# Optimization experiments

Hardware: AMD Instinct MI355X
Metric: run time of the kernel (lower is better)

The kernel has to match this reference:

```python
import jax, jax.numpy as jnp
import numpy as np

VX, VY, VT = 3.0, 3.0, 1.0
PCX, PCY, PCT = 346.0, 260.0, 200.0
GX, GY = 116, 87  # ceil(346/3), ceil(260/3)
B = 4
NSEG = B * GX * GY  # dense pillar id space (replaces torch.unique)
EPS = 1e-3  # BatchNorm1d eps


def _bn_swish(h, gamma, beta):
    # BatchNorm1d (training-mode batch stats) + Swish
    mu = jnp.mean(h, axis=0)
    var = jnp.var(h, axis=0)
    h = (h - mu) * jax.lax.rsqrt(var + EPS) * gamma + beta
    return h * jax.nn.sigmoid(h)


def _voxelize(points):
    # points: [N,5] = (batch_idx, x, y, t, polarity)
    cx = jnp.floor(points[:, 1] / VX).astype(jnp.int32)
    cy = jnp.floor(points[:, 2] / VY).astype(jnp.int32)
    bi = points[:, 0].astype(jnp.int32)
    inv = (bi * GX + cx) * GY + cy  # dense pillar id == unq_inv into dense grid
    xyz = points[:, 1:4]
    cnt = jax.ops.segment_sum(jnp.ones_like(xyz[:, 0]), inv, num_segments=NSEG)
    mean = jax.ops.segment_sum(xyz, inv, num_segments=NSEG) / jnp.maximum(cnt, 1.0)[:, None]
    f_cluster = xyz - mean[inv]
    cxy = jnp.stack([cx, cy], axis=1).astype(points.dtype)
    vsz = jnp.array([VX, VY], points.dtype)
    f_center = points[:, 1:3] - (cxy * vsz + (vsz - 1.0) / 2.0)
    feats = jnp.concatenate([points[:, 1:5], f_cluster, f_center], axis=1)  # [N,9]
    scale = jnp.array([PCX, PCY, PCT, 1.0, VX, VY, PCT, VX, VY], points.dtype)
    feats = feats / scale
    return feats[:, :4], inv, cnt  # module only keeps first 4 feature columns


def _resize_bilinear_ac(x, Ho, Wo):
    # F.interpolate(mode='bilinear', align_corners=True)
    _, _, H, W = x.shape
    ys = jnp.linspace(0.0, H - 1.0, Ho)
    xs = jnp.linspace(0.0, W - 1.0, Wo)
    y0 = jnp.floor(ys).astype(jnp.int32); y1 = jnp.minimum(y0 + 1, H - 1)
    x0 = jnp.floor(xs).astype(jnp.int32); x1 = jnp.minimum(x0 + 1, W - 1)
    wy = (ys - y0.astype(x.dtype))[None, None, :, None]
    wx = (xs - x0.astype(x.dtype))[None, None, None, :]
    xh = x[:, :, y0, :] * (1.0 - wy) + x[:, :, y1, :] * wy
    return xh[:, :, :, x0] * (1.0 - wx) + xh[:, :, :, x1] * wx


def setup_inputs() -> dict:
    key = jax.random.key(0)
    ks = jax.random.split(key, 8)
    N = 1_000_000
    b = jax.random.randint(ks[0], (N, 1), 0, B).astype(jnp.float32)
    x = jax.random.uniform(ks[1], (N, 1)) * 345.9
    y = jax.random.uniform(ks[2], (N, 1)) * 259.9
    t = jax.random.uniform(ks[3], (N, 1)) * 199.9
    p = jax.random.randint(ks[4], (N, 1), 0, 2).astype(jnp.float32)
    points = jnp.concatenate([b, x, y, t, p], axis=1)
    fus = jax.random.normal(ks[5], (B, 3, 224, 224), jnp.float32)
    W0 = jax.random.normal(ks[6], (4, 32), jnp.float32) * 0.1
    g0 = jnp.ones(32, jnp.float32); b0 = jnp.zeros(32, jnp.float32)
    W1 = jax.random.normal(ks[7], (64, 128), jnp.float32) * 0.05
    g1 = jnp.ones(128, jnp.float32); b1 = jnp.zeros(128, jnp.float32)
    return {"fus": fus, "points": points, "W0": W0, "g0": g0, "b0": b0,
            "W1": W1, "g1": g1, "b1": b1}


def reference(fus, points, W0, g0, b0, W1, g1, b1):
    feats, inv, cnt = _voxelize(points)
    # PFNLayer 0 (not last): units = 64//2 = 32, concat per-pillar max
    h0 = _bn_swish(feats @ W0, g0, b0)
    m0 = jax.ops.segment_max(h0, inv, num_segments=NSEG)
    x1 = jnp.concatenate([h0, m0[inv]], axis=1)  # [N,64]
    # PFNLayer 1 (last): units = 128, returns broadcast per-pillar max
    h1 = _bn_swish(x1 @ W1, g1, b1)
    m1 = jax.ops.segment_max(h1, inv, num_segments=NSEG)  # [NSEG,128]
    # final scatter_max over the broadcast max equals m1 on occupied pillars;
    # spconv .dense() zero-fills empty pillars
    occ = cnt > 0
    dense = jnp.where(occ[:, None], m1, 0.0)
    dense = dense.reshape(B, GX, GY, -1).transpose(0, 3, 2, 1)  # [B,C,GY,GX]
    return _resize_bilinear_ac(dense, 224, 224)
```

## Files before the change

kernel.cpp:

```cpp
#include <hip/hip_runtime.h>
#include <cmath>

#define NPTS   1000000
#define GXD    116
#define GYD    87
#define NB     4
#define NSEG   40368
#define OUTN   25690112

#define OFF_INV    0
#define OFF_CNT    2000000
#define OFF_OFFS   2050000
#define OFF_FILL   2100000
#define OFF_STATS  2150000
#define OFF_BN0    2158500
#define OFF_FRAG   2158592
#define OFF_MINP   2170000
#define OFF_MAXP   7340000
#define OFF_SPTS   12510000

typedef __attribute__((ext_vector_type(8))) short short8v;
typedef __attribute__((ext_vector_type(4))) float float4v;

union Frag {
  unsigned u[4];
  int4 i4;
  short8v v;
};

__device__ __forceinline__ float fastrcp(float x) { return __builtin_amdgcn_rcpf(x); }
__device__ __forceinline__ float swishf(float z) { return z * fastrcp(1.0f + __expf(-z)); }
__device__ __forceinline__ unsigned fbits(float x) { return __builtin_bit_cast(unsigned, x); }
__device__ __forceinline__ float ubf(unsigned x) { return __builtin_bit_cast(float, x); }

__device__ __forceinline__ void bfsplit2(float x0, float x1, unsigned& hi, unsigned& lo) {
  unsigned h0b = fbits(x0) & 0xffff0000u;
  unsigned h1b = fbits(x1) & 0xffff0000u;
  hi = (h0b >> 16) | h1b;
  float l0 = x0 - ubf(h0b), l1 = x1 - ubf(h1b);
  lo = (fbits(l0) >> 16) | (fbits(l1) & 0xffff0000u);
}

__global__ __launch_bounds__(256) void k_init(int* __restrict__ cnt, int* __restrict__ fill,
                                              float* __restrict__ stats) {
  int i = blockIdx.x * 256 + threadIdx.x;
  if (i < NSEG) { cnt[i] = 0; fill[i] = 0; }
  if (i < 8224) stats[i] = 0.0f;
}

__global__ __launch_bounds__(256) void k_point1(const float* __restrict__ pts,
                                                int* __restrict__ inv,
                                                int* __restrict__ cnt,
                                                float* __restrict__ Sg) {
  float acc[14];
  #pragma unroll
  for (int q = 0; q < 14; ++q) acc[q] = 0.0f;
  const float i346 = 1.0f / 346.0f, i260 = 1.0f / 260.0f, i200 = 1.0f / 200.0f;
  const int stride = gridDim.x * 256;
  for (int i = blockIdx.x * 256 + threadIdx.x; i < NPTS; i += stride) {
    float b = pts[i*5];
    float4 v = *(const float4*)(pts + i*5 + 1);
    float x = v.x, y = v.y, t = v.z, p = v.w;
    int cx = (int)floorf(x / 3.0f);
    int cy = (int)floorf(y / 3.0f);
    int bi = (int)b;
    if (cx >= 0 && cx < GXD && cy >= 0 && cy < GYD && bi >= 0 && bi < NB) {
      int iv = (bi*GXD + cx)*GYD + cy;
      inv[i] = iv;
      atomicAdd(&cnt[iv], 1);
    } else {
      inv[i] = -1;
    }
    float f0 = x*i346, f1 = y*i260, f2 = t*i200, f3 = p;
    acc[0]+=f0; acc[1]+=f1; acc[2]+=f2; acc[3]+=f3;
    acc[4]+=f0*f0; acc[5]+=f0*f1; acc[6]+=f0*f2; acc[7]+=f0*f3;
    acc[8]+=f1*f1; acc[9]+=f1*f2; acc[10]+=f1*f3;
    acc[11]+=f2*f2; acc[12]+=f2*f3; acc[13]+=f3*f3;
  }
  __shared__ float lds[4*14];
  int lane = threadIdx.x & 63, wave = threadIdx.x >> 6;
  #pragma unroll
  for (int q = 0; q < 14; ++q) {
    float v = acc[q];
    #pragma unroll
    for (int d = 32; d > 0; d >>= 1) v += __shfl_down(v, d, 64);
    if (lane == 0) lds[wave*14 + q] = v;
  }
  __syncthreads();
  if (threadIdx.x < 14) {
    float v = lds[threadIdx.x] + lds[14+threadIdx.x] + lds[28+threadIdx.x] + lds[42+threadIdx.x];
    atomicAdd(&Sg[threadIdx.x], v);
  }
}

__global__ __launch_bounds__(1024) void k_scan(const int* __restrict__ cnt,
                                               int* __restrict__ offs,
                                               const float* __restrict__ S,
                                               float* __restrict__ bn0,
                                               int4* __restrict__ frag,
                                               const float* __restrict__ W0,
                                               const float* __restrict__ g0,
                                               const float* __restrict__ b0,
                                               const float* __restrict__ W1) {
  __shared__ int wtot[16];
  const int tid = threadIdx.x;
  if (tid < 32) {
    const float invN = 1.0f / (float)NPTS;
    float w0 = W0[tid], w1 = W0[32+tid], w2 = W0[64+tid], w3 = W0[96+tid];
    float mu = (S[0]*w0 + S[1]*w1 + S[2]*w2 + S[3]*w3) * invN;
    float e2 = (S[4]*w0*w0 + S[8]*w1*w1 + S[11]*w2*w2 + S[13]*w3*w3
              + 2.0f*(S[5]*w0*w1 + S[6]*w0*w2 + S[7]*w0*w3
                    + S[9]*w1*w2 + S[10]*w1*w3 + S[12]*w2*w3)) * invN;
    float var = e2 - mu*mu;
    float a = rsqrtf(var + 1e-3f) * g0[tid];
    bn0[tid] = a;
    bn0[32+tid] = b0[tid] - mu*a;
  }
  if (tid < 512) {
    const int t = tid >> 6, ln = tid & 63;
    const int qq = ln >> 4, rr = ln & 15;
    Frag fh, fl, gh, gl;
    #pragma unroll
    for (int d = 0; d < 4; ++d) {
      int row = 8*qq + 2*d, col = 16*t + rr;
      bfsplit2(W1[row*128 + col],      W1[(row+1)*128 + col],  fh.u[d], fl.u[d]);
      bfsplit2(W1[(32+row)*128 + col], W1[(33+row)*128 + col], gh.u[d], gl.u[d]);
    }
    frag[tid]        = fh.i4;
    frag[512 + tid]  = fl.i4;
    frag[1024 + tid] = gh.i4;
    frag[1536 + tid] = gl.i4;
  }
  const int CH = 40;
  const int base = tid * CH;
  int loc[CH];
  int s = 0;
  #pragma unroll
  for (int i = 0; i < CH; ++i) {
    int v = (base + i < NSEG) ? cnt[base + i] : 0;
    loc[i] = s; s += v;
  }
  int inc = s;
  const int lane = tid & 63, wv = tid >> 6;
  #pragma unroll
  for (int d = 1; d < 64; d <<= 1) {
    int t = __shfl_up(inc, d, 64);
    if (lane >= d) inc += t;
  }
  if (lane == 63) wtot[wv] = inc;
  __syncthreads();
  if (tid == 0) {
    int run = 0;
    #pragma unroll
    for (int w = 0; w < 16; ++w) { int t = wtot[w]; wtot[w] = run; run += t; }
    offs[NSEG] = run;
  }
  __syncthreads();
  int ex = wtot[wv] + (inc - s);
  #pragma unroll
  for (int i = 0; i < CH; ++i)
    if (base + i < NSEG) offs[base + i] = ex + loc[i];
}

__global__ __launch_bounds__(256) void k_scatter(const float* __restrict__ pts,
                                                 const int* __restrict__ inv,
                                                 const int* __restrict__ offs,
                                                 int* __restrict__ fill,
                                                 float4* __restrict__ sp) {
  int i = blockIdx.x * 256 + threadIdx.x;
  if (i >= NPTS) return;
  int iv = inv[i];
  if (iv < 0) return;
  float4 v = *(const float4*)(pts + i*5 + 1);
  int pos = offs[iv] + atomicAdd(&fill[iv], 1);
  sp[pos] = v;
}

__global__ __launch_bounds__(256) void k_seg(const float4* __restrict__ sp,
                                             const int* __restrict__ offs,
                                             const float* __restrict__ W0,
                                             const float* __restrict__ bn0,
                                             const int4* __restrict__ frags,
                                             float* __restrict__ minp,
                                             float* __restrict__ maxp,
                                             float* __restrict__ stats) {
  __shared__ int4 fragLDS[1536];
  __shared__ float redS[4][16][16];
  const int tid = threadIdx.x;
  const int wave = tid >> 6, lane = tid & 63;
  const int q = lane >> 4, r = lane & 15;

  short8v Bhi[8];
  #pragma unroll
  for (int t = 0; t < 8; ++t) {
    Frag f; f.i4 = frags[t*64 + lane];
    Bhi[t] = f.v;
  }
  for (int i = tid; i < 1536; i += 256) fragLDS[i] = frags[512 + i];

  const float i346 = 1.0f/346.0f, i260 = 1.0f/260.0f, i200 = 1.0f/200.0f;
  float wax[8], way[8], wat[8], wap[8], wc0[8];
  #pragma unroll
  for (int j = 0; j < 8; ++j) {
    int ch = 8*q + j;
    float a0 = bn0[ch];
    wax[j] = W0[ch]    * (i346 * a0);
    way[j] = W0[32+ch] * (i260 * a0);
    wat[j] = W0[64+ch] * (i200 * a0);
    wap[j] = W0[96+ch] * a0;
    wc0[j] = bn0[32+ch];
  }
  __syncthreads();

  float gsum[8], gssq[8];
  #pragma unroll
  for (int t = 0; t < 8; ++t) { gsum[t] = 0.f; gssq[t] = 0.f; }

  const int w = blockIdx.x*4 + wave;
  const int qn = NSEG >> 13;
  const int rm = NSEG - (qn << 13);
  const int s0 = w*qn + (w < rm ? w : rm);
  const int scnt = qn + (w < rm ? 1 : 0);

  for (int s = s0; s < s0 + scnt; ++s) {
    const int off = offs[s], pend = offs[s+1];
    const int n = pend - off;
    if (n <= 0) continue;
    const int ngroups = (n + 15) >> 4;
    float m0r[8], mn[8], mx[8], su[8], sq[8];
    #pragma unroll
    for (int t = 0; t < 8; ++t) {
      m0r[t] = -1e30f; mn[t] = 1e30f; mx[t] = -1e30f; su[t] = 0.f; sq[t] = 0.f;
    }
    float4 P = sp[off + (r < n ? r : 0)];
    for (int g = 0; g < ngroups; ++g) {
      int slot1 = (g+1)*16 + r;
      float4 Pn = sp[off + (slot1 < n ? slot1 : 0)];

      float h0v[8];
      #pragma unroll
      for (int j = 0; j < 8; ++j) {
        float pre = fmaf(P.x, wax[j], fmaf(P.y, way[j], fmaf(P.z, wat[j], fmaf(P.w, wap[j], wc0[j]))));
        float h = swishf(pre);
        h0v[j] = h;
        m0r[j] = fmaxf(m0r[j], h);
      }
      Frag ah, al;
      #pragma unroll
      for (int d = 0; d < 4; ++d)
        bfsplit2(h0v[2*d], h0v[2*d+1], ah.u[d], al.u[d]);

      const int rem = n - g*16;
      #pragma unroll
      for (int t = 0; t < 8; ++t) {
        Frag fb; fb.i4 = fragLDS[t*64 + lane];
        float4v acc = {0.f, 0.f, 0.f, 0.f};
        acc = __builtin_amdgcn_mfma_f32_16x16x32_bf16(ah.v, Bhi[t], acc, 0, 0, 0);
        acc = __builtin_amdgcn_mfma_f32_16x16x32_bf16(ah.v, fb.v,   acc, 0, 0, 0);
        acc = __builtin_amdgcn_mfma_f32_16x16x32_bf16(al.v, Bhi[t], acc, 0, 0, 0);
        if (rem >= 16) {
          #pragma unroll
          for (int i = 0; i < 4; ++i) {
            float z = acc[i];
            mn[t] = fminf(mn[t], z); mx[t] = fmaxf(mx[t], z);
            su[t] += z; sq[t] = fmaf(z, z, sq[t]);
          }
        } else {
          #pragma unroll
          for (int i = 0; i < 4; ++i) {
            float z = acc[i];
            mn[t] = fminf(mn[t], z); mx[t] = fmaxf(mx[t], z);
            float zz = (4*q + i < rem) ? z : 0.f;
            su[t] += zz; sq[t] = fmaf(zz, zz, sq[t]);
          }
        }
      }
      P = Pn;
    }

    #pragma unroll
    for (int j = 0; j < 8; ++j) {
      float v = m0r[j];
      v = fmaxf(v, __shfl_xor(v, 1, 64));
      v = fmaxf(v, __shfl_xor(v, 2, 64));
      v = fmaxf(v, __shfl_xor(v, 4, 64));
      v = fmaxf(v, __shfl_xor(v, 8, 64));
      m0r[j] = v;
    }
    Frag mh, ml;
    #pragma unroll
    for (int d = 0; d < 4; ++d)
      bfsplit2(m0r[2*d], m0r[2*d+1], mh.u[d], ml.u[d]);
    float c[8];
    #pragma unroll
    for (int t = 0; t < 8; ++t) {
      Frag gh; gh.i4 = fragLDS[512 + t*64 + lane];
      Frag gl; gl.i4 = fragLDS[1024 + t*64 + lane];
      float4v cacc = {0.f, 0.f, 0.f, 0.f};
      cacc = __builtin_amdgcn_mfma_f32_16x16x32_bf16(mh.v, gh.v, cacc, 0, 0, 0);
      cacc = __builtin_amdgcn_mfma_f32_16x16x32_bf16(mh.v, gl.v, cacc, 0, 0, 0);
      cacc = __builtin_amdgcn_mfma_f32_16x16x32_bf16(ml.v, gh.v, cacc, 0, 0, 0);
      c[t] = cacc[0];
    }
    #pragma unroll
    for (int t = 0; t < 8; ++t) {
      mn[t] = fminf(mn[t], __shfl_xor(mn[t], 16, 64));
      mn[t] = fminf(mn[t], __shfl_xor(mn[t], 32, 64));
      mx[t] = fmaxf(mx[t], __shfl_xor(mx[t], 16, 64));
      mx[t] = fmaxf(mx[t], __shfl_xor(mx[t], 32, 64));
      su[t] += __shfl_xor(su[t], 16, 64);
      su[t] += __shfl_xor(su[t], 32, 64);
      sq[t] += __shfl_xor(sq[t], 16, 64);
      sq[t] += __shfl_xor(sq[t], 32, 64);
      float nf = (float)n;
      gsum[t] += su[t] + nf * c[t];
      gssq[t] += sq[t] + 2.0f*c[t]*su[t] + nf*c[t]*c[t];
    }
    if (lane < 16) {
      #pragma unroll
      for (int t = 0; t < 8; ++t) {
        minp[(16*t + r)*NSEG + s] = mn[t] + c[t];
        maxp[(16*t + r)*NSEG + s] = mx[t] + c[t];
      }
    }
  }
  if (lane < 16) {
    #pragma unroll
    for (int t = 0; t < 8; ++t) {
      redS[wave][r][t]     = gsum[t];
      redS[wave][r][8 + t] = gssq[t];
    }
  }
  __syncthreads();
  if (wave == 0 && lane < 16) {
    const int cpy = blockIdx.x & 15;
    float* sb = stats + 16 + 512*cpy;
    #pragma unroll
    for (int t = 0; t < 8; ++t) {
      float s0v = redS[0][r][t]   + redS[1][r][t]   + redS[2][r][t]   + redS[3][r][t];
      float q0v = redS[0][r][8+t] + redS[1][r][8+t] + redS[2][r][8+t] + redS[3][r][8+t];
      atomicAdd(&sb[16*t + r], s0v);
      atomicAdd(&sb[256 + 16*t + r], q0v);
    }
  }
}

__global__ __launch_bounds__(256) void k_plane(const float* __restrict__ minp,
                                               const float* __restrict__ maxp,
                                               const int* __restrict__ offs,
                                               const float* __restrict__ stats,
                                               const float* __restrict__ g1,
                                               const float* __restrict__ b1,
                                               float* __restrict__ out) {
  __shared__ float plane[87*117];
  __shared__ float ab[2];
  const int c = blockIdx.x & 127;
  const int b = blockIdx.x >> 7;
  const int tid = threadIdx.x;
  if (tid == 0) {
    float s = 0.f, q2 = 0.f;
    #pragma unroll
    for (int cpy = 0; cpy < 16; ++cpy) {
      s  += stats[16 + 512*cpy + c];
      q2 += stats[16 + 512*cpy + 256 + c];
    }
    const float invN = 1.0f / (float)NPTS;
    float mu = s * invN;
    float var = q2 * invN - mu*mu;
    float a = rsqrtf(var + 1e-3f) * g1[c];
    ab[0] = a;
    ab[1] = b1[c] - mu*a;
  }
  __syncthreads();
  const float a = ab[0], bb = ab[1];
  const int sBase = b * (GXD*GYD);
  const float* mnp = minp + c*NSEG + sBase;
  const float* mxp = maxp + c*NSEG + sBase;
  for (int i = tid; i < GXD*GYD; i += 256) {
    int gx = i / GYD, gy = i - gx*GYD;
    float m = 0.0f;
    int s = sBase + i;
    if (offs[s+1] - offs[s] > 0) {
      float zl = fmaf(a, mnp[i], bb);
      float zh = fmaf(a, mxp[i], bb);
      m = fmaxf(swishf(zl), swishf(zh));
    }
    plane[gy*117 + gx] = m;
  }
  __syncthreads();
  float* op = out + (size_t)blockIdx.x * (224*224);
  for (int o4 = tid; o4 < 224*56; o4 += 256) {
    int xq = o4 % 56;
    int yo = o4 / 56;
    float ys = (float)yo * (86.0f/223.0f);
    float yf = floorf(ys); int y0 = (int)yf; int y1 = min(y0+1, 86); float wy = ys - yf;
    const float* p0 = plane + y0*117;
    const float* p1 = plane + y1*117;
    float res[4];
    #pragma unroll
    for (int gph = 0; gph < 4; ++gph) {
      int xo = xq*4 + gph;
      float xs = (float)xo * (115.0f/223.0f);
      float xf = floorf(xs); int x0 = (int)xf; int x1 = min(x0+1, 115); float wx = xs - xf;
      float c0v = p0[x0]*(1.0f-wy) + p1[x0]*wy;
      float c1v = p0[x1]*(1.0f-wy) + p1[x1]*wy;
      res[gph] = c0v*(1.0f-wx) + c1v*wx;
    }
    *(float4*)&op[yo*224 + xq*4] = make_float4(res[0], res[1], res[2], res[3]);
  }
}

extern "C" void kernel_launch(void* const* d_in, const int* in_sizes, int n_in,
                              void* d_out, int out_size, void* d_ws, size_t ws_size,
                              hipStream_t stream) {
  const float* pts = (const float*)d_in[1];
  const float* W0  = (const float*)d_in[2];
  const float* g0  = (const float*)d_in[3];
  const float* b0  = (const float*)d_in[4];
  const float* W1  = (const float*)d_in[5];
  const float* g1  = (const float*)d_in[6];
  const float* b1  = (const float*)d_in[7];
  float* out = (float*)d_out;
  int*   wsi = (int*)d_ws;
  float* wsf = (float*)d_ws;

  k_init<<<158, 256, 0, stream>>>(wsi+OFF_CNT, wsi+OFF_FILL, wsf+OFF_STATS);
  k_point1<<<256, 256, 0, stream>>>(pts, wsi+OFF_INV, wsi+OFF_CNT, wsf+OFF_STATS);
  k_scan<<<1, 1024, 0, stream>>>(wsi+OFF_CNT, wsi+OFF_OFFS, wsf+OFF_STATS, wsf+OFF_BN0,
                                 (int4*)(wsf+OFF_FRAG), W0, g0, b0, W1);
  k_scatter<<<(NPTS+255)/256, 256, 0, stream>>>(pts, wsi+OFF_INV, wsi+OFF_OFFS,
                                                wsi+OFF_FILL, (float4*)(wsf+OFF_SPTS));
  k_seg<<<2048, 256, 0, stream>>>((const float4*)(wsf+OFF_SPTS), wsi+OFF_OFFS, W0,
                                  wsf+OFF_BN0, (const int4*)(wsf+OFF_FRAG),
                                  wsf+OFF_MINP, wsf+OFF_MAXP, wsf+OFF_STATS);
  k_plane<<<NB*128, 256, 0, stream>>>(wsf+OFF_MINP, wsf+OFF_MAXP, wsi+OFF_OFFS,
                                      wsf+OFF_STATS, g1, b1, out);
}
```

Baseline: 430.9 us.

## Stage per-segment min/max in LDS and write contiguous runs; use min3/max3

The segment kernel now hands each block a contiguous range of segments, with its four waves interleaved across that range, instead of giving each wave its own contiguous range. Per-segment min/max results are staged in shared memory and then written cooperatively, so stores into the channel-major min/max planes form contiguous runs instead of scattered single-element writes. Grid size doubles to 4096 blocks. The statistic accumulation uses v_min3/v_max3 inline asm and pairwise sums, which changes the order of float additions slightly.

Result: slower. 458.0 us (+6.3%).

```diff
diff --git a/kernel.cpp b/kernel.cpp
--- a/kernel.cpp
+++ b/kernel.cpp
@@ -7,6 +7,9 @@
 #define NB     4
 #define NSEG   40368
 #define OUTN   25690112
+
+#define SEGBLK 4096
+#define CHUNKMAX 10
 
 #define OFF_INV    0
 #define OFF_CNT    2000000
@@ -32,6 +35,13 @@
 __device__ __forceinline__ float swishf(float z) { return z * fastrcp(1.0f + __expf(-z)); }
 __device__ __forceinline__ unsigned fbits(float x) { return __builtin_bit_cast(unsigned, x); }
 __device__ __forceinline__ float ubf(unsigned x) { return __builtin_bit_cast(float, x); }
+
+__device__ __forceinline__ float min3f(float a, float b, float c) {
+  float d; asm("v_min3_f32 %0, %1, %2, %3" : "=v"(d) : "v"(a), "v"(b), "v"(c)); return d;
+}
+__device__ __forceinline__ float max3f(float a, float b, float c) {
+  float d; asm("v_max3_f32 %0, %1, %2, %3" : "=v"(d) : "v"(a), "v"(b), "v"(c)); return d;
+}
 
 __device__ __forceinline__ void bfsplit2(float x0, float x1, unsigned& hi, unsigned& lo) {
   unsigned h0b = fbits(x0) & 0xffff0000u;
@@ -186,6 +196,8 @@
                                              float* __restrict__ stats) {
   __shared__ int4 fragLDS[1536];
   __shared__ float redS[4][16][16];
+  __shared__ float mnT[CHUNKMAX][129];
+  __shared__ float mxT[CHUNKMAX][129];
   const int tid = threadIdx.x;
   const int wave = tid >> 6, lane = tid & 63;
   const int q = lane >> 4, r = lane & 15;
@@ -216,13 +228,13 @@
   #pragma unroll
   for (int t = 0; t < 8; ++t) { gsum[t] = 0.f; gssq[t] = 0.f; }
 
-  const int w = blockIdx.x*4 + wave;
-  const int qn = NSEG >> 13;
-  const int rm = NSEG - (qn << 13);
-  const int s0 = w*qn + (w < rm ? w : rm);
-  const int scnt = qn + (w < rm ? 1 : 0);
-
-  for (int s = s0; s < s0 + scnt; ++s) {
+  const int bq = NSEG / SEGBLK;
+  const int br = NSEG - bq*SEGBLK;
+  const int S0 = blockIdx.x*bq + min((int)blockIdx.x, br);
+  const int csz = bq + (blockIdx.x < br ? 1 : 0);
+
+  for (int si = wave; si < csz; si += 4) {
+    const int s = S0 + si;
     const int off = offs[s], pend = offs[s+1];
     const int n = pend - off;
     if (n <= 0) continue;
@@ -258,21 +270,23 @@
         acc = __builtin_amdgcn_mfma_f32_16x16x32_bf16(ah.v, Bhi[t], acc, 0, 0, 0);
         acc = __builtin_amdgcn_mfma_f32_16x16x32_bf16(ah.v, fb.v,   acc, 0, 0, 0);
         acc = __builtin_amdgcn_mfma_f32_16x16x32_bf16(al.v, Bhi[t], acc, 0, 0, 0);
+        float z0 = acc[0], z1 = acc[1], z2 = acc[2], z3 = acc[3];
         if (rem >= 16) {
-          #pragma unroll
-          for (int i = 0; i < 4; ++i) {
-            float z = acc[i];
-            mn[t] = fminf(mn[t], z); mx[t] = fmaxf(mx[t], z);
-            su[t] += z; sq[t] = fmaf(z, z, sq[t]);
-          }
+          mn[t] = min3f(z0, z1, min3f(z2, z3, mn[t]));
+          mx[t] = max3f(z0, z1, max3f(z2, z3, mx[t]));
+          su[t] += (z0 + z1) + (z2 + z3);
+          sq[t] = fmaf(z0, z0, sq[t]); sq[t] = fmaf(z1, z1, sq[t]);
+          sq[t] = fmaf(z2, z2, sq[t]); sq[t] = fmaf(z3, z3, sq[t]);
         } else {
-          #pragma unroll
-          for (int i = 0; i < 4; ++i) {
-            float z = acc[i];
-            mn[t] = fminf(mn[t], z); mx[t] = fmaxf(mx[t], z);
-            float zz = (4*q + i < rem) ? z : 0.f;
-            su[t] += zz; sq[t] = fmaf(zz, zz, sq[t]);
-          }
+          mn[t] = min3f(z0, z1, min3f(z2, z3, mn[t]));
+          mx[t] = max3f(z0, z1, max3f(z2, z3, mx[t]));
+          float zz0 = (4*q + 0 < rem) ? z0 : 0.f;
+          float zz1 = (4*q + 1 < rem) ? z1 : 0.f;
+          float zz2 = (4*q + 2 < rem) ? z2 : 0.f;
+          float zz3 = (4*q + 3 < rem) ? z3 : 0.f;
+          su[t] += (zz0 + zz1) + (zz2 + zz3);
+          sq[t] = fmaf(zz0, zz0, sq[t]); sq[t] = fmaf(zz1, zz1, sq[t]);
+          sq[t] = fmaf(zz2, zz2, sq[t]); sq[t] = fmaf(zz3, zz3, sq[t]);
         }
       }
       P = Pn;
@@ -319,11 +333,12 @@
     if (lane < 16) {
       #pragma unroll
       for (int t = 0; t < 8; ++t) {
-        minp[(16*t + r)*NSEG + s] = mn[t] + c[t];
-        maxp[(16*t + r)*NSEG + s] = mx[t] + c[t];
+        mnT[si][16*t + r] = mn[t] + c[t];
+        mxT[si][16*t + r] = mx[t] + c[t];
       }
     }
   }
+
   if (lane < 16) {
     #pragma unroll
     for (int t = 0; t < 8; ++t) {
@@ -332,6 +347,12 @@
     }
   }
   __syncthreads();
+
+  for (int i = tid; i < (csz << 7); i += 256) {
+    int ch = i / csz, si = i - ch*csz;
+    minp[ch*NSEG + S0 + si] = mnT[si][ch];
+    maxp[ch*NSEG + S0 + si] = mxT[si][ch];
+  }
   if (wave == 0 && lane < 16) {
     const int cpy = blockIdx.x & 15;
     float* sb = stats + 16 + 512*cpy;
@@ -430,9 +451,9 @@
                                  (int4*)(wsf+OFF_FRAG), W0, g0, b0, W1);
   k_scatter<<<(NPTS+255)/256, 256, 0, stream>>>(pts, wsi+OFF_INV, wsi+OFF_OFFS,
                                                 wsi+OFF_FILL, (float4*)(wsf+OFF_SPTS));
-  k_seg<<<2048, 256, 0, stream>>>((const float4*)(wsf+OFF_SPTS), wsi+OFF_OFFS, W0,
-                                  wsf+OFF_BN0, (const int4*)(wsf+OFF_FRAG),
-                                  wsf+OFF_MINP, wsf+OFF_MAXP, wsf+OFF_STATS);
+  k_seg<<<SEGBLK, 256, 0, stream>>>((const float4*)(wsf+OFF_SPTS), wsi+OFF_OFFS, W0,
+                                    wsf+OFF_BN0, (const int4*)(wsf+OFF_FRAG),
+                                    wsf+OFF_MINP, wsf+OFF_MAXP, wsf+OFF_STATS);
   k_plane<<<NB*128, 256, 0, stream>>>(wsf+OFF_MINP, wsf+OFF_MAXP, wsi+OFF_OFFS,
                                       wsf+OFF_STATS, g1, b1, out);
 }
```
